# Kernel tuning notes

Hardware: AMD Instinct MI355X
Metric: run time of the kernel (lower is better)

## Reference

```python
import jax, jax.numpy as jnp
import numpy as np

B, T, C = 2, 2048, 1024
NH = 16
HS = C // NH

def setup_inputs() -> dict:
    key = jax.random.key(0)
    ks = jax.random.split(key, 5)
    x = jax.random.normal(ks[0], (B, T, C), dtype=jnp.float32)
    scale = 1.0 / np.sqrt(C)
    Wk = jax.random.normal(ks[1], (C, C), dtype=jnp.float32) * scale
    bk = jax.random.normal(ks[2], (C,), dtype=jnp.float32) * scale
    Wv = jax.random.normal(ks[3], (C, C), dtype=jnp.float32) * scale
    bv = jax.random.normal(ks[4], (C,), dtype=jnp.float32) * scale
    return {"x": x, "Wk": Wk, "bk": bk, "Wv": Wv, "bv": bv}

def reference(x, Wk, bk, Wv, bv):
    b, t, c = x.shape
    # projections: key and value are Dense; query is identity (as in source)
    k = (x @ Wk + bk).reshape(b, t, NH, HS).transpose(0, 2, 1, 3)  # b nh T hs
    q = x.reshape(b, t, NH, HS).transpose(0, 2, 1, 3)              # b nh T hs
    v = (x @ Wv + bv).reshape(b, t, NH, HS).transpose(0, 2, 1, 3)  # b nh T hs
    # NOTE: source computes logits = K @ Q^T (no 1/sqrt(d) scaling)
    logits = jnp.einsum('bhid,bhjd->bhij', k, q)                   # b nh T T
    causal = jnp.tril(jnp.ones((t, t), dtype=bool))                # True where allowed
    masked = jnp.where(causal[None, None, :, :], logits, -jnp.inf)
    att = jax.nn.softmax(masked, axis=-1)
    y = jnp.einsum('bhij,bhjd->bhid', att, v)                      # b nh T hs
    return y.transpose(0, 2, 1, 3).reshape(b, t, c)
```

## Files before the change

kernel.cpp:

```cpp
#include <hip/hip_runtime.h>
#include <cstdint>
#include <cstddef>

#define BB  2
#define TT  2048
#define CC  1024
#define NHH 16
#define HSS 64
#define BT  (BB*TT)

typedef unsigned short u16;
typedef unsigned int u32;
typedef _Float16 f16;
typedef __attribute__((ext_vector_type(8))) _Float16 f16x8;
typedef __attribute__((ext_vector_type(8))) __bf16 bf16x8;
typedef __attribute__((ext_vector_type(4))) float f32x4;

__device__ __forceinline__ u16 f2bf(float f) {
    union { float f; u32 u; } x; x.f = f;
    return (u16)((x.u + 0x7fffu + ((x.u >> 16) & 1u)) >> 16);
}
__device__ __forceinline__ u16 f2h(float f) {
    union { f16 h; u16 u; } x; x.h = (f16)f;
    return x.u;
}

#define MFMA_BF(a,b,c) __builtin_amdgcn_mfma_f32_16x16x32_bf16((a),(b),(c),0,0,0)
#define MFMA_F16(a,b,c) __builtin_amdgcn_mfma_f32_16x16x32_f16((a),(b),(c),0,0,0)

__device__ __forceinline__ void gld16(const u16* g, u16* l) {
    __builtin_amdgcn_global_load_lds(
        (const __attribute__((address_space(1))) unsigned int*)g,
        (__attribute__((address_space(3))) unsigned int*)l, 16, 0, 0);
}

__global__ __launch_bounds__(256) void convert_x(
    const float* __restrict__ X, u16* __restrict__ Xf)
{
    const int idx = (blockIdx.x * 256 + threadIdx.x) * 8;
    const float4 a = *(const float4*)&X[idx];
    const float4 b = *(const float4*)&X[idx + 4];
    float v[8] = {a.x, a.y, a.z, a.w, b.x, b.y, b.z, b.w};
    union { uint4 u; u16 s[8]; } H;
    #pragma unroll
    for (int u = 0; u < 8; ++u) H.s[u] = f2h(v[u]);
    *(uint4*)&Xf[idx] = H.u;
}

__global__ __launch_bounds__(256) void convert_w(
    const float* __restrict__ Wk, const float* __restrict__ Wv,
    u16* __restrict__ WkT, u16* __restrict__ WvT)
{
    const bool isK = (blockIdx.z == 0);
    const float* W = isK ? Wk : Wv;
    u16* WT = isK ? WkT : WvT;
    __shared__ __align__(16) u16 LH[64][72];
    const int tid = threadIdx.x;
    const int k0 = blockIdx.y * 64, n0 = blockIdx.x * 64;
    {
        const int row = tid >> 2, coff = (tid & 3) * 16;
        const float* g = &W[(size_t)(k0 + row) * CC + n0 + coff];
        #pragma unroll
        for (int u = 0; u < 16; ++u) LH[row][coff + u] = f2h(g[u]);
    }
    __syncthreads();
    {
        const int n = tid >> 2, kc = (tid & 3) * 16;
        union { uint4 u[2]; u16 s[16]; } Hq;
        #pragma unroll
        for (int u = 0; u < 16; ++u) Hq.s[u] = LH[kc + u][n];
        uint4* ph = (uint4*)&WT[(size_t)(n0 + n) * CC + k0 + kc];
        ph[0] = Hq.u[0]; ph[1] = Hq.u[1];
    }
}

__global__ __launch_bounds__(256) void proj_kernel(
    const u16* __restrict__ Xf, const u16* __restrict__ WkT,
    const u16* __restrict__ WvT,
    const float* __restrict__ bk, const float* __restrict__ bv,
    u16* __restrict__ Kf, u16* __restrict__ Vt)
{
    const bool isK = (blockIdx.z == 0);
    const u16* WT = isK ? WkT : WvT;

    __shared__ u16 Ah[128 * 64], Bh[128 * 64];

    const int tid = threadIdx.x;
    const int m0 = blockIdx.y * 128, n0 = blockIdx.x * 128;
    const int w = tid >> 6, lane = tid & 63;
    const int quad = lane >> 4, l15 = lane & 15;
    const int wm = (w >> 1) * 64, wn = (w & 1) * 64;

    f32x4 acc[4][4] = {};

    for (int k0 = 0; k0 < CC; k0 += 64) {
        const u16* src = (w < 2) ? Xf : WT;
        u16* dst = (w < 2) ? Ah : Bh;
        const int rb = (w < 2) ? m0 : n0;
        #pragma unroll
        for (int t = 0; t < 8; ++t) {
            int ci = (w & 1) * 512 + t * 64 + lane;
            int r = ci >> 3, cp = ci & 7;
            int cg = (cp - r) & 7;
            gld16(src + (size_t)(rb + r) * CC + k0 + cg * 8,
                  dst + ((w & 1) * 512 + t * 64) * 8);
        }
        __syncthreads();

        #pragma unroll
        for (int kk = 0; kk < 2; ++kk) {
            f16x8 ah[4];
            #pragma unroll
            for (int i = 0; i < 4; ++i) {
                const int row = wm + i * 16 + l15;
                const int cp = ((kk * 4 + quad + row) & 7) * 8;
                ah[i] = *(const f16x8*)&Ah[row * 64 + cp];
            }
            #pragma unroll
            for (int j = 0; j < 4; ++j) {
                const int rowb = wn + j * 16 + l15;
                const int cpb = ((kk * 4 + quad + rowb) & 7) * 8;
                f16x8 bh_ = *(const f16x8*)&Bh[rowb * 64 + cpb];
                #pragma unroll
                for (int i = 0; i < 4; ++i)
                    acc[i][j] = MFMA_F16(ah[i], bh_, acc[i][j]);
            }
        }
        __syncthreads();
    }

    if (isK) {
        #pragma unroll
        for (int j = 0; j < 4; ++j) {
            const int col = n0 + wn + j * 16 + l15;
            const float bias = bk[col];
            #pragma unroll
            for (int i = 0; i < 4; ++i) {
                const int rowb = m0 + wm + i * 16 + quad * 4;
                #pragma unroll
                for (int r = 0; r < 4; ++r)
                    Kf[(size_t)(rowb + r) * CC + col] = f2h(acc[i][j][r] + bias);
            }
        }
    } else {
        #pragma unroll
        for (int j = 0; j < 4; ++j) {
            const int col = n0 + wn + j * 16 + l15;
            const float bias = bv[col];
            const int d = col & (HSS - 1), hh = col >> 6;
            #pragma unroll
            for (int i = 0; i < 4; ++i) {
                const int t0 = m0 + wm + i * 16 + quad * 4;
                const int bb = t0 >> 11, tt = t0 & (TT - 1);
                ushort4 pk;
                pk.x = f2bf(acc[i][j][0] + bias);
                pk.y = f2bf(acc[i][j][1] + bias);
                pk.z = f2bf(acc[i][j][2] + bias);
                pk.w = f2bf(acc[i][j][3] + bias);
                *(ushort4*)&Vt[((size_t)(bb * NHH + hh) * HSS + d) * TT + tt] = pk;
            }
        }
    }
}

__global__ __launch_bounds__(256) void attn_kernel(
    const u16* __restrict__ Xf, const u16* __restrict__ Kf,
    const u16* __restrict__ Vt, float* __restrict__ out)
{
    const int L = blockIdx.x;
    const int tile_r = (L >> 3) & 31;
    const int grp = L >> 8;
    const int hb = (L & 7) + 8 * grp;
    const int it = 31 - tile_r;
    const int h = hb & (NHH - 1), b = hb >> 4;
    const int i0 = it * 64;

    __shared__ __align__(16) u16 Xs[64][72];
    __shared__ __align__(16) u16 Vs[64][72];
    __shared__ __align__(16) u16 Ps[4][16][72];

    const int tid = threadIdx.x;
    const int w = tid >> 6, lane = tid & 63;
    const int quad = lane >> 4, l15 = lane & 15;
    const size_t rowbase = (size_t)b * TT;
    const int hd = h * HSS;
    const size_t vgbase = (size_t)(b * NHH + h) * HSS * TT;

    bf16x8 ones;
    { union { u32 u[4]; bf16x8 v; } o;
      #pragma unroll
      for (int i = 0; i < 4; ++i) o.u[i] = 0x3F803F80u;
      ones = o.v; }

    f16x8 qf[2];
    #pragma unroll
    for (int c = 0; c < 2; ++c)
        qf[c] = *(const f16x8*)&Kf[(rowbase + i0 + w * 16 + l15) * CC + hd + c * 32 + quad * 8];

    float4 dummy; (void)dummy;
    f32x4 o_[4] = {};
    f32x4 lacc = {};

    const int jj0 = tid >> 3, df0 = (tid & 7) * 8;
    const int jj1 = (tid + 256) >> 3, df1 = ((tid + 256) & 7) * 8;
    uint4 pX0, pX1, pV0, pV1;

    pX0 = *(const uint4*)&Xf[(rowbase + jj0) * CC + hd + df0];
    pX1 = *(const uint4*)&Xf[(rowbase + jj1) * CC + hd + df1];
    pV0 = *(const uint4*)&Vt[vgbase + (size_t)jj0 * TT + df0];
    pV1 = *(const uint4*)&Vt[vgbase + (size_t)jj1 * TT + df1];

    for (int jt = 0; jt <= it; ++jt) {
        *(uint4*)&Xs[jj0][df0] = pX0;
        *(uint4*)&Xs[jj1][df1] = pX1;
        *(uint4*)&Vs[jj0][df0] = pV0;
        *(uint4*)&Vs[jj1][df1] = pV1;
        __syncthreads();

        if (jt < it) {
            const int j0n = (jt + 1) * 64;
            pX0 = *(const uint4*)&Xf[(rowbase + j0n + jj0) * CC + hd + df0];
            pX1 = *(const uint4*)&Xf[(rowbase + j0n + jj1) * CC + hd + df1];
            pV0 = *(const uint4*)&Vt[vgbase + (size_t)jj0 * TT + j0n + df0];
            pV1 = *(const uint4*)&Vt[vgbase + (size_t)jj1 * TT + j0n + df1];
        }

        f32x4 s[4];
        #pragma unroll
        for (int nt = 0; nt < 4; ++nt) {
            const int krow = nt * 16 + l15;
            f16x8 xb0 = *(const f16x8*)&Xs[krow][quad * 8];
            f16x8 xb1 = *(const f16x8*)&Xs[krow][32 + quad * 8];
            f32x4 z = {};
            z = MFMA_F16(qf[0], xb0, z);
            z = MFMA_F16(qf[1], xb1, z);
            s[nt] = z;
        }
        if (jt == it) {
            #pragma unroll
            for (int nt = 0; nt < 4; ++nt) {
                const int jg = nt * 16 + l15;
                #pragma unroll
                for (int r = 0; r < 4; ++r)
                    if (jg > w * 16 + quad * 4 + r) s[nt][r] = -1e30f;
            }
        }

        #pragma unroll
        for (int nt = 0; nt < 4; ++nt)
            #pragma unroll
            for (int r = 0; r < 4; ++r)
                Ps[w][quad * 4 + r][nt * 16 + l15] = f2bf(__expf(s[nt][r] - 20.f));

        bf16x8 ap0 = *(const bf16x8*)&Ps[w][l15][quad * 8];
        bf16x8 ap1 = *(const bf16x8*)&Ps[w][l15][32 + quad * 8];

        lacc = MFMA_BF(ap0, ones, lacc);
        lacc = MFMA_BF(ap1, ones, lacc);

        #pragma unroll
        for (int dt = 0; dt < 4; ++dt) {
            bf16x8 bv0 = *(const bf16x8*)&Vs[dt * 16 + l15][quad * 8];
            bf16x8 bv1 = *(const bf16x8*)&Vs[dt * 16 + l15][32 + quad * 8];
            o_[dt] = MFMA_BF(ap0, bv0, o_[dt]);
            o_[dt] = MFMA_BF(ap1, bv1, o_[dt]);
        }
        __syncthreads();
    }

    float linv[4];
    #pragma unroll
    for (int r = 0; r < 4; ++r) linv[r] = 1.f / lacc[r];
    #pragma unroll
    for (int dt = 0; dt < 4; ++dt) {
        #pragma unroll
        for (int r = 0; r < 4; ++r) {
            const int ig = i0 + w * 16 + quad * 4 + r;
            out[(rowbase + ig) * CC + hd + dt * 16 + l15] = o_[dt][r] * linv[r];
        }
    }
}

extern "C" void kernel_launch(void* const* d_in, const int* in_sizes, int n_in,
                              void* d_out, int out_size, void* d_ws, size_t ws_size,
                              hipStream_t stream) {
    (void)in_sizes; (void)n_in; (void)out_size; (void)ws_size;
    const float* x  = (const float*)d_in[0];
    const float* Wk = (const float*)d_in[1];
    const float* bk = (const float*)d_in[2];
    const float* Wv = (const float*)d_in[3];
    const float* bv = (const float*)d_in[4];
    float* out = (float*)d_out;

    const size_t M4 = (size_t)BT * CC;
    const size_t M1 = (size_t)CC * CC;
    u16* Xf  = (u16*)d_ws;
    u16* Kf  = Xf + M4;
    u16* Vt  = Kf + M4;
    u16* WkT = Vt + M4;
    u16* WvT = WkT + M1;

    convert_x<<<dim3(M4 / (256 * 8)), 256, 0, stream>>>(x, Xf);
    convert_w<<<dim3(16, 16, 2), 256, 0, stream>>>(Wk, Wv, WkT, WvT);
    proj_kernel<<<dim3(8, 32, 2), 256, 0, stream>>>(
        Xf, WkT, WvT, bk, bv, Kf, Vt);
    attn_kernel<<<dim3(1024), 256, 0, stream>>>(Xf, Kf, Vt, out);
}
```

Before: 170.1 us.

## Double-buffer GEMM and attention loads, pair causal tiles, stage epilogue stores via LDS

```diff
diff --git a/kernel.cpp b/kernel.cpp
--- a/kernel.cpp
+++ b/kernel.cpp
@@ -80,33 +80,54 @@
     const float* __restrict__ bk, const float* __restrict__ bv,
     u16* __restrict__ Kf, u16* __restrict__ Vt)
 {
-    const bool isK = (blockIdx.z == 0);
+    __shared__ u16 SM[4][8192];
+
+    const int id = blockIdx.x;
+    const int xcd = id & 7, idx = id >> 3;
+    const int z = idx >> 5, rem = idx & 31;
+    const int n0 = (rem & 7) * 128;
+    const int m0 = (xcd * 4 + (rem >> 3)) * 128;
+    const bool isK = (z == 0);
     const u16* WT = isK ? WkT : WvT;
 
-    __shared__ u16 Ah[128 * 64], Bh[128 * 64];
-
     const int tid = threadIdx.x;
-    const int m0 = blockIdx.y * 128, n0 = blockIdx.x * 128;
     const int w = tid >> 6, lane = tid & 63;
     const int quad = lane >> 4, l15 = lane & 15;
     const int wm = (w >> 1) * 64, wn = (w & 1) * 64;
 
+    const u16* src = (w < 2) ? Xf : WT;
+    const int rb = (w < 2) ? m0 : n0;
+    int srow[8], scg[8];
+    #pragma unroll
+    for (int t = 0; t < 8; ++t) {
+        int ci = (w & 1) * 512 + t * 64 + lane;
+        srow[t] = ci >> 3;
+        scg[t] = ((ci & 7) - srow[t]) & 7;
+    }
+    const int sbase = (w & 1) * 4096;
+
     f32x4 acc[4][4] = {};
 
-    for (int k0 = 0; k0 < CC; k0 += 64) {
-        const u16* src = (w < 2) ? Xf : WT;
-        u16* dst = (w < 2) ? Ah : Bh;
-        const int rb = (w < 2) ? m0 : n0;
-        #pragma unroll
-        for (int t = 0; t < 8; ++t) {
-            int ci = (w & 1) * 512 + t * 64 + lane;
-            int r = ci >> 3, cp = ci & 7;
-            int cg = (cp - r) & 7;
-            gld16(src + (size_t)(rb + r) * CC + k0 + cg * 8,
-                  dst + ((w & 1) * 512 + t * 64) * 8);
-        }
+    {
+        u16* dst = ((w < 2) ? SM[0] : SM[2]) + sbase;
+        #pragma unroll
+        for (int t = 0; t < 8; ++t)
+            gld16(src + (size_t)(rb + srow[t]) * CC + scg[t] * 8, dst + t * 512);
+    }
+
+    for (int ki = 0; ki < 16; ++ki) {
+        const int buf = ki & 1;
         __syncthreads();
-
+        if (ki < 15) {
+            u16* dst = ((w < 2) ? SM[buf ^ 1] : SM[2 + (buf ^ 1)]) + sbase;
+            const int k0n = (ki + 1) * 64;
+            #pragma unroll
+            for (int t = 0; t < 8; ++t)
+                gld16(src + (size_t)(rb + srow[t]) * CC + k0n + scg[t] * 8,
+                      dst + t * 512);
+        }
+        const u16* Ab = SM[buf];
+        const u16* Bb = SM[2 + buf];
         #pragma unroll
         for (int kk = 0; kk < 2; ++kk) {
             f16x8 ah[4];
@@ -114,52 +135,62 @@
             for (int i = 0; i < 4; ++i) {
                 const int row = wm + i * 16 + l15;
                 const int cp = ((kk * 4 + quad + row) & 7) * 8;
-                ah[i] = *(const f16x8*)&Ah[row * 64 + cp];
+                ah[i] = *(const f16x8*)&Ab[row * 64 + cp];
             }
             #pragma unroll
             for (int j = 0; j < 4; ++j) {
                 const int rowb = wn + j * 16 + l15;
                 const int cpb = ((kk * 4 + quad + rowb) & 7) * 8;
-                f16x8 bh_ = *(const f16x8*)&Bh[rowb * 64 + cpb];
+                f16x8 bh_ = *(const f16x8*)&Bb[rowb * 64 + cpb];
                 #pragma unroll
                 for (int i = 0; i < 4; ++i)
                     acc[i][j] = MFMA_F16(ah[i], bh_, acc[i][j]);
             }
         }
+    }
+
+    __syncthreads();
+    u16* XL = &SM[0][0];
+
+    if (isK) {
+        #pragma unroll
+        for (int j = 0; j < 4; ++j) {
+            const float bias = bk[n0 + wn + j * 16 + l15];
+            #pragma unroll
+            for (int i = 0; i < 4; ++i)
+                #pragma unroll
+                for (int r = 0; r < 4; ++r)
+                    XL[(wm + i * 16 + quad * 4 + r) * 136 + wn + j * 16 + l15] =
+                        f2h(acc[i][j][r] + bias);
+        }
         __syncthreads();
-    }
-
-    if (isK) {
+        const int r = tid >> 1, half = tid & 1;
+        #pragma unroll
+        for (int t = 0; t < 8; ++t)
+            *(uint4*)&Kf[(size_t)(m0 + r) * CC + n0 + half * 64 + t * 8] =
+                *(const uint4*)&XL[r * 136 + half * 64 + t * 8];
+    } else {
         #pragma unroll
         for (int j = 0; j < 4; ++j) {
-            const int col = n0 + wn + j * 16 + l15;
-            const float bias = bk[col];
+            const float bias = bv[n0 + wn + j * 16 + l15];
             #pragma unroll
             for (int i = 0; i < 4; ++i) {
-                const int rowb = m0 + wm + i * 16 + quad * 4;
-                #pragma unroll
-                for (int r = 0; r < 4; ++r)
-                    Kf[(size_t)(rowb + r) * CC + col] = f2h(acc[i][j][r] + bias);
-            }
-        }
-    } else {
-        #pragma unroll
-        for (int j = 0; j < 4; ++j) {
-            const int col = n0 + wn + j * 16 + l15;
-            const float bias = bv[col];
-            const int d = col & (HSS - 1), hh = col >> 6;
-            #pragma unroll
-            for (int i = 0; i < 4; ++i) {
-                const int t0 = m0 + wm + i * 16 + quad * 4;
-                const int bb = t0 >> 11, tt = t0 & (TT - 1);
-                ushort4 pk;
-                pk.x = f2bf(acc[i][j][0] + bias);
-                pk.y = f2bf(acc[i][j][1] + bias);
-                pk.z = f2bf(acc[i][j][2] + bias);
-                pk.w = f2bf(acc[i][j][3] + bias);
-                *(ushort4*)&Vt[((size_t)(bb * NHH + hh) * HSS + d) * TT + tt] = pk;
-            }
-        }
+                uint2 pk;
+                pk.x = (u32)f2bf(acc[i][j][0] + bias) |
+                       ((u32)f2bf(acc[i][j][1] + bias) << 16);
+                pk.y = (u32)f2bf(acc[i][j][2] + bias) |
+                       ((u32)f2bf(acc[i][j][3] + bias) << 16);
+                *(uint2*)&XL[(wn + j * 16 + l15) * 136 + wm + i * 16 + quad * 4] = pk;
+            }
+        }
+        __syncthreads();
+        const int nl = tid >> 1, half = tid & 1;
+        const int d = (n0 + nl) & (HSS - 1), hh = (n0 + nl) >> 6;
+        const int bb = m0 >> 11, tb = (m0 & (TT - 1)) + half * 64;
+        const size_t gb = ((size_t)(bb * NHH + hh) * HSS + d) * TT + tb;
+        #pragma unroll
+        for (int t = 0; t < 8; ++t)
+            *(uint4*)&Vt[gb + t * 8] = *(const uint4*)&XL[nl * 136 + half * 64 + t * 8];
     }
 }
 
@@ -167,17 +198,16 @@
     const u16* __restrict__ Xf, const u16* __restrict__ Kf,
     const u16* __restrict__ Vt, float* __restrict__ out)
 {
+    __shared__ u16 Xs[2][4096];
+    __shared__ u16 Vs[2][4096];
+    __shared__ __align__(16) u16 Ps[4][2][1152];
+
     const int L = blockIdx.x;
-    const int tile_r = (L >> 3) & 31;
-    const int grp = L >> 8;
-    const int hb = (L & 7) + 8 * grp;
-    const int it = 31 - tile_r;
+    const int xcd = L & 7, k = (L >> 3) & 15, grp = L >> 7;
+    const int hb = xcd + 8 * grp;
     const int h = hb & (NHH - 1), b = hb >> 4;
-    const int i0 = it * 64;
-
-    __shared__ __align__(16) u16 Xs[64][72];
-    __shared__ __align__(16) u16 Vs[64][72];
-    __shared__ __align__(16) u16 Ps[4][16][72];
+    const int iA = k, iB = 31 - k;
+    const int i0A = iA * 64, i0B = iB * 64;
 
     const int tid = threadIdx.x;
     const int w = tid >> 6, lane = tid & 63;
@@ -192,57 +222,83 @@
       for (int i = 0; i < 4; ++i) o.u[i] = 0x3F803F80u;
       ones = o.v; }
 
-    f16x8 qf[2];
-    #pragma unroll
-    for (int c = 0; c < 2; ++c)
-        qf[c] = *(const f16x8*)&Kf[(rowbase + i0 + w * 16 + l15) * CC + hd + c * 32 + quad * 8];
-
-    float4 dummy; (void)dummy;
-    f32x4 o_[4] = {};
-    f32x4 lacc = {};
-
-    const int jj0 = tid >> 3, df0 = (tid & 7) * 8;
-    const int jj1 = (tid + 256) >> 3, df1 = ((tid + 256) & 7) * 8;
-    uint4 pX0, pX1, pV0, pV1;
-
-    pX0 = *(const uint4*)&Xf[(rowbase + jj0) * CC + hd + df0];
-    pX1 = *(const uint4*)&Xf[(rowbase + jj1) * CC + hd + df1];
-    pV0 = *(const uint4*)&Vt[vgbase + (size_t)jj0 * TT + df0];
-    pV1 = *(const uint4*)&Vt[vgbase + (size_t)jj1 * TT + df1];
-
-    for (int jt = 0; jt <= it; ++jt) {
-        *(uint4*)&Xs[jj0][df0] = pX0;
-        *(uint4*)&Xs[jj1][df1] = pX1;
-        *(uint4*)&Vs[jj0][df0] = pV0;
-        *(uint4*)&Vs[jj1][df1] = pV1;
+    f16x8 qA[2], qB[2];
+    #pragma unroll
+    for (int c = 0; c < 2; ++c) {
+        qA[c] = *(const f16x8*)&Kf[(rowbase + i0A + w * 16 + l15) * CC + hd + c * 32 + quad * 8];
+        qB[c] = *(const f16x8*)&Kf[(rowbase + i0B + w * 16 + l15) * CC + hd + c * 32 + quad * 8];
+    }
+
+    int crow[2], ccg[2], cbase[2];
+    #pragma unroll
+    for (int t = 0; t < 2; ++t) {
+        const int ci = t * 256 + tid;
+        crow[t] = ci >> 3;
+        ccg[t] = ((ci & 7) - crow[t]) & 7;
+        cbase[t] = (t * 256 + w * 64) * 8;
+    }
+    const u16* gx[2]; const u16* gv[2];
+    #pragma unroll
+    for (int t = 0; t < 2; ++t) {
+        gx[t] = Xf + (rowbase + crow[t]) * CC + hd + ccg[t] * 8;
+        gv[t] = Vt + vgbase + (size_t)crow[t] * TT + ccg[t] * 8;
+    }
+
+    #pragma unroll
+    for (int t = 0; t < 2; ++t) {
+        gld16(gx[t], Xs[0] + cbase[t]);
+        gld16(gv[t], Vs[0] + cbase[t]);
+    }
+
+    f32x4 oA[4] = {}, oB[4] = {};
+    f32x4 laA = {}, laB = {};
+
+    for (int jt = 0; jt <= iB; ++jt) {
+        const int buf = jt & 1;
         __syncthreads();
-
-        if (jt < it) {
+        if (jt < iB) {
             const int j0n = (jt + 1) * 64;
-            pX0 = *(const uint4*)&Xf[(rowbase + j0n + jj0) * CC + hd + df0];
-            pX1 = *(const uint4*)&Xf[(rowbase + j0n + jj1) * CC + hd + df1];
-            pV0 = *(const uint4*)&Vt[vgbase + (size_t)jj0 * TT + j0n + df0];
-            pV1 = *(const uint4*)&Vt[vgbase + (size_t)jj1 * TT + j0n + df1];
-        }
-
-        f32x4 s[4];
+            #pragma unroll
+            for (int t = 0; t < 2; ++t) {
+                gld16(gx[t] + (size_t)j0n * CC, Xs[buf ^ 1] + cbase[t]);
+                gld16(gv[t] + j0n, Vs[buf ^ 1] + cbase[t]);
+            }
+        }
+        const bool doA = (jt <= iA);
+
+        f32x4 sB[4], sA[4];
         #pragma unroll
         for (int nt = 0; nt < 4; ++nt) {
             const int krow = nt * 16 + l15;
-            f16x8 xb0 = *(const f16x8*)&Xs[krow][quad * 8];
-            f16x8 xb1 = *(const f16x8*)&Xs[krow][32 + quad * 8];
+            f16x8 x0 = *(const f16x8*)&Xs[buf][krow * 64 + ((quad + krow) & 7) * 8];
+            f16x8 x1 = *(const f16x8*)&Xs[buf][krow * 64 + ((quad + 4 + krow) & 7) * 8];
             f32x4 z = {};
-            z = MFMA_F16(qf[0], xb0, z);
-            z = MFMA_F16(qf[1], xb1, z);
-            s[nt] = z;
-        }
-        if (jt == it) {
+            z = MFMA_F16(qB[0], x0, z);
+            z = MFMA_F16(qB[1], x1, z);
+            sB[nt] = z;
+            if (doA) {
+                f32x4 y = {};
+                y = MFMA_F16(qA[0], x0, y);
+                y = MFMA_F16(qA[1], x1, y);
+                sA[nt] = y;
+            }
+        }
+        if (jt == iB) {
             #pragma unroll
             for (int nt = 0; nt < 4; ++nt) {
                 const int jg = nt * 16 + l15;
                 #pragma unroll
                 for (int r = 0; r < 4; ++r)
-                    if (jg > w * 16 + quad * 4 + r) s[nt][r] = -1e30f;
+                    if (jg > w * 16 + quad * 4 + r) sB[nt][r] = -1e30f;
+            }
+        }
+        if (doA && jt == iA) {
+            #pragma unroll
+            for (int nt = 0; nt < 4; ++nt) {
+                const int jg = nt * 16 + l15;
+                #pragma unroll
+                for (int r = 0; r < 4; ++r)
+                    if (jg > w * 16 + quad * 4 + r) sA[nt][r] = -1e30f;
             }
         }
 
@@ -250,33 +306,54 @@
         for (int nt = 0; nt < 4; ++nt)
             #pragma unroll
             for (int r = 0; r < 4; ++r)
-                Ps[w][quad * 4 + r][nt * 16 + l15] = f2bf(__expf(s[nt][r] - 20.f));
-
-        bf16x8 ap0 = *(const bf16x8*)&Ps[w][l15][quad * 8];
-        bf16x8 ap1 = *(const bf16x8*)&Ps[w][l15][32 + quad * 8];
-
-        lacc = MFMA_BF(ap0, ones, lacc);
-        lacc = MFMA_BF(ap1, ones, lacc);
+                Ps[w][0][(quad * 4 + r) * 72 + nt * 16 + l15] =
+                    f2bf(__expf(sB[nt][r] - 20.f));
+        if (doA) {
+            #pragma unroll
+            for (int nt = 0; nt < 4; ++nt)
+                #pragma unroll
+                for (int r = 0; r < 4; ++r)
+                    Ps[w][1][(quad * 4 + r) * 72 + nt * 16 + l15] =
+                        f2bf(__expf(sA[nt][r] - 20.f));
+        }
+
+        bf16x8 aB0 = *(const bf16x8*)&Ps[w][0][l15 * 72 + quad * 8];
+        bf16x8 aB1 = *(const bf16x8*)&Ps[w][0][l15 * 72 + 32 + quad * 8];
+        laB = MFMA_BF(aB0, ones, laB);
+        laB = MFMA_BF(aB1, ones, laB);
+        bf16x8 aA0, aA1;
+        if (doA) {
+            aA0 = *(const bf16x8*)&Ps[w][1][l15 * 72 + quad * 8];
+            aA1 = *(const bf16x8*)&Ps[w][1][l15 * 72 + 32 + quad * 8];
+            laA = MFMA_BF(aA0, ones, laA);
+            laA = MFMA_BF(aA1, ones, laA);
+        }
 
         #pragma unroll
         for (int dt = 0; dt < 4; ++dt) {
-            bf16x8 bv0 = *(const bf16x8*)&Vs[dt * 16 + l15][quad * 8];
-            bf16x8 bv1 = *(const bf16x8*)&Vs[dt * 16 + l15][32 + quad * 8];
-            o_[dt] = MFMA_BF(ap0, bv0, o_[dt]);
-            o_[dt] = MFMA_BF(ap1, bv1, o_[dt]);
-        }
-        __syncthreads();
-    }
-
-    float linv[4];
-    #pragma unroll
-    for (int r = 0; r < 4; ++r) linv[r] = 1.f / lacc[r];
+            const int vrow = dt * 16 + l15;
+            bf16x8 v0 = *(const bf16x8*)&Vs[buf][vrow * 64 + ((quad + vrow) & 7) * 8];
+            bf16x8 v1 = *(const bf16x8*)&Vs[buf][vrow * 64 + ((quad + 4 + vrow) & 7) * 8];
+            oB[dt] = MFMA_BF(aB0, v0, oB[dt]);
+            oB[dt] = MFMA_BF(aB1, v1, oB[dt]);
+            if (doA) {
+                oA[dt] = MFMA_BF(aA0, v0, oA[dt]);
+                oA[dt] = MFMA_BF(aA1, v1, oA[dt]);
+            }
+        }
+    }
+
+    float liA[4], liB[4];
+    #pragma unroll
+    for (int r = 0; r < 4; ++r) { liA[r] = 1.f / laA[r]; liB[r] = 1.f / laB[r]; }
     #pragma unroll
     for (int dt = 0; dt < 4; ++dt) {
         #pragma unroll
         for (int r = 0; r < 4; ++r) {
-            const int ig = i0 + w * 16 + quad * 4 + r;
-            out[(rowbase + ig) * CC + hd + dt * 16 + l15] = o_[dt][r] * linv[r];
+            const int igA = i0A + w * 16 + quad * 4 + r;
+            const int igB = i0B + w * 16 + quad * 4 + r;
+            out[(rowbase + igA) * CC + hd + dt * 16 + l15] = oA[dt][r] * liA[r];
+            out[(rowbase + igB) * CC + hd + dt * 16 + l15] = oB[dt][r] * liB[r];
         }
     }
 }
@@ -302,7 +379,6 @@
 
     convert_x<<<dim3(M4 / (256 * 8)), 256, 0, stream>>>(x, Xf);
     convert_w<<<dim3(16, 16, 2), 256, 0, stream>>>(Wk, Wv, WkT, WvT);
-    proj_kernel<<<dim3(8, 32, 2), 256, 0, stream>>>(
-        Xf, WkT, WvT, bk, bv, Kf, Vt);
-    attn_kernel<<<dim3(1024), 256, 0, stream>>>(Xf, Kf, Vt, out);
-}
+    proj_kernel<<<dim3(512), 256, 0, stream>>>(Xf, WkT, WvT, bk, bv, Kf, Vt);
+    attn_kernel<<<dim3(512), 256, 0, stream>>>(Xf, Kf, Vt, out);
+}
```

Result: faster. 154.2 us (-9.3%).
